# Optimization experiments

Measured on AMD Instinct MI355X. Metric: run time of the kernel, lower is better.

## Reference

```python
import jax, jax.numpy as jnp
import numpy as np

P = 64
K = 64
D = 2048
KERNEL_MUL = 2.0
KERNEL_NUM = 5


def setup_inputs() -> dict:
    key = jax.random.key(0)
    k1, k2 = jax.random.split(key)
    source = jax.random.normal(k1, (P * K, D), dtype=jnp.float32)
    target = jax.random.normal(k2, (P * K, D), dtype=jnp.float32)
    return {"source": source, "target": target}


def _mmd_terms(source, target):
    # split into P groups of K rows each, process all splits at once
    src = source.reshape(P, K, D)
    tgt = target.reshape(P, K, D)
    total = jnp.concatenate([src, tgt], axis=1)          # [P, 2K, D]
    n = 2 * K
    # pairwise squared L2 distances per split: [P, 2K, 2K]
    sq = jnp.sum(total * total, axis=-1)                  # [P, 2K]
    gram = jnp.einsum('pid,pjd->pij', total, total)       # [P, 2K, 2K]
    l2 = sq[:, :, None] + sq[:, None, :] - 2.0 * gram
    # bandwidth from detached distances (torch uses L2_distance.data)
    bw = jax.lax.stop_gradient(jnp.sum(l2, axis=(1, 2))) / (n * n - n)  # [P]
    bw = bw / (KERNEL_MUL ** (KERNEL_NUM // 2))
    mults = KERNEL_MUL ** jnp.arange(KERNEL_NUM, dtype=jnp.float32)     # [kn]
    bws = bw[:, None] * mults[None, :] + 1e-9                           # [P, kn]
    # multi-bandwidth Gaussian kernel sum: [P, 2K, 2K]
    kern = jnp.sum(jnp.exp(-l2[:, None, :, :] / bws[:, :, None, None]), axis=1)
    XX = kern[:, :K, :K]
    YY = kern[:, K:, K:]
    XY = kern[:, :K, K:]
    YX = kern[:, K:, :K]
    xx = jnp.mean(XX, axis=(1, 2))
    yy = jnp.mean(YY, axis=(1, 2))
    xy = jnp.mean(XY, axis=(1, 2))
    yx = jnp.mean(YX, axis=(1, 2))
    per_split_loss = xx + yy - xy - yx                    # [P]
    total_loss = jnp.sum(per_split_loss) / P
    return total_loss, l2, xx, yy, xy, yx


def reference(source, target):
    total_loss, l2, xx, yy, xy, yx = _mmd_terms(source, target)
    # original returns max of l2dist from the LAST split only
    max_l2_last = jnp.max(l2[-1])
    return (total_loss.reshape(1), max_l2_last,
            jnp.sum(xx) / P, jnp.sum(yy) / P, jnp.sum(xy) / P, jnp.sum(yx) / P)
```

## Files before the change

kernel.cpp:

```cpp
#include <hip/hip_runtime.h>

typedef _Float16 half8 __attribute__((ext_vector_type(8)));
typedef _Float16 half4v __attribute__((ext_vector_type(4)));
typedef float floatx4 __attribute__((ext_vector_type(4)));
typedef unsigned int uint2v __attribute__((ext_vector_type(2)));

#define NSPLIT 64
#define KS 64
#define DIM 2048
#define NROW 128
#define BK 128
#define KSPL 4
#define KCH (DIM / KSPL)
#define NKC_A (KCH / BK)
#define SST 152
#define GSZ (NROW * NROW)
#define NBLK (NSPLIT * KSPL)
#define GT2F_OFF (NBLK * GSZ / 2)
#define PART_OFF (GT2F_OFF + NBLK)
#define FLAG_OFF (PART_OFF + NBLK * 4)


__device__ __forceinline__ unsigned int pk16(float a, float b) {
  return __builtin_bit_cast(unsigned int, __builtin_amdgcn_cvt_pkrtz(a, b));
}

__global__ __launch_bounds__(1024) void gram_kernel(const float* __restrict__ src,
                                                    const float* __restrict__ tgt,
                                                    float* __restrict__ ws) {
  __shared__ __align__(16) _Float16 stage[NROW * SST];
  __shared__ float red[16];

  const int p = blockIdx.x >> 2;
  const int c = blockIdx.x & (KSPL - 1);
  const int tid = threadIdx.x;
  const int lane = tid & 63;
  const int wave = tid >> 6;

  const int srow = tid >> 3;
  const int c4 = (tid & 7) * 4;
  const float* rowp = ((srow < KS) ? (src + (size_t)(p * KS + srow) * DIM)
                                   : (tgt + (size_t)(p * KS + (srow - KS)) * DIM)) +
                      c * KCH;

  const int wr = (wave >> 2) * 32;
  const int wc = (wave & 3) * 32;
  const int fr = lane & 15;
  const int fk = (lane >> 4) * 8;

  floatx4 acc00 = {0.f, 0.f, 0.f, 0.f};
  floatx4 acc01 = {0.f, 0.f, 0.f, 0.f};
  floatx4 acc10 = {0.f, 0.f, 0.f, 0.f};
  floatx4 acc11 = {0.f, 0.f, 0.f, 0.f};

  float4 f0, f1, f2, f3;
#define LOADK(kc)                                      \
  do {                                                 \
    const float* gp_ = rowp + (kc) * BK + c4;          \
    f0 = *(const float4*)(gp_);                        \
    f1 = *(const float4*)(gp_ + 32);                   \
    f2 = *(const float4*)(gp_ + 64);                   \
    f3 = *(const float4*)(gp_ + 96);                   \
  } while (0)

  LOADK(0);
  for (int kc = 0; kc < NKC_A; ++kc) {
    __syncthreads();
    {
      _Float16* sp = &stage[srow * SST + c4];
      *(uint2v*)(sp)      = (uint2v){pk16(f0.x, f0.y), pk16(f0.z, f0.w)};
      *(uint2v*)(sp + 32) = (uint2v){pk16(f1.x, f1.y), pk16(f1.z, f1.w)};
      *(uint2v*)(sp + 64) = (uint2v){pk16(f2.x, f2.y), pk16(f2.z, f2.w)};
      *(uint2v*)(sp + 96) = (uint2v){pk16(f3.x, f3.y), pk16(f3.z, f3.w)};
    }
    __syncthreads();
    if (kc + 1 < NKC_A) LOADK(kc + 1);
#pragma unroll
    for (int ks = 0; ks < 4; ++ks) {
      const int ko = ks * 32 + fk;
      half8 a0 = *(const half8*)&stage[(wr + fr) * SST + ko];
      half8 a1 = *(const half8*)&stage[(wr + 16 + fr) * SST + ko];
      half8 b0 = *(const half8*)&stage[(wc + fr) * SST + ko];
      half8 b1 = *(const half8*)&stage[(wc + 16 + fr) * SST + ko];
      acc00 = __builtin_amdgcn_mfma_f32_16x16x32_f16(a0, b0, acc00, 0, 0, 0);
      acc01 = __builtin_amdgcn_mfma_f32_16x16x32_f16(a0, b1, acc01, 0, 0, 0);
      acc10 = __builtin_amdgcn_mfma_f32_16x16x32_f16(a1, b0, acc10, 0, 0, 0);
      acc11 = __builtin_amdgcn_mfma_f32_16x16x32_f16(a1, b1, acc11, 0, 0, 0);
    }
  }
#undef LOADK

  _Float16* hs = (_Float16*)ws + (size_t)blockIdx.x * GSZ + wave * 1024 + lane * 4;
  {
    half4v h0, h1, h2, h3;
#pragma unroll
    for (int r = 0; r < 4; ++r) {
      h0[r] = (_Float16)acc00[r];
      h1[r] = (_Float16)acc01[r];
      h2[r] = (_Float16)acc10[r];
      h3[r] = (_Float16)acc11[r];
    }
    *(half4v*)(hs)       = h0;
    *(half4v*)(hs + 256) = h1;
    *(half4v*)(hs + 512) = h2;
    *(half4v*)(hs + 768) = h3;
  }

  float gsum = 0.0f;
#pragma unroll
  for (int r = 0; r < 4; ++r) gsum += acc00[r] + acc01[r] + acc10[r] + acc11[r];
#pragma unroll
  for (int m = 1; m <= 32; m <<= 1) gsum += __shfl_xor(gsum, m, 64);
  if (lane == 0) red[wave] = gsum;
  __syncthreads();
  if (tid == 0) {
    float t = 0.0f;
    for (int w = 0; w < 16; ++w) t += red[w];
    ws[GT2F_OFF + blockIdx.x] = t;
  }
}

__global__ __launch_bounds__(1024) void reduce_kernel(float* __restrict__ ws,
                                                      float* __restrict__ out) {
  __shared__ float sqv[NROW];
  __shared__ float bcast[8];
  __shared__ float redm[16];
  __shared__ float quad2[2];
  __shared__ float fr2[4][5];
  __shared__ int sh_go;

  const int b = blockIdx.x;
  const int p = b >> 2;
  const int rb = b & 3;
  const int tid = threadIdx.x;
  const int lane = tid & 63;
  const int wave = tid >> 6;
  int* iflag = (int*)(ws + FLAG_OFF);

  const int row = rb * 32 + (tid >> 5);
  const int cg = tid & 31;

  const _Float16* sb = (const _Float16*)ws + (size_t)(p * KSPL) * GSZ;
  const int wv = ((row >> 5) << 2) + (cg >> 3);
  const int a = (((row >> 4) & 1) << 1) + ((cg >> 2) & 1);
  const int ln = (((row & 15) >> 2) << 4) + ((cg & 3) << 2);
  const int idx = wv * 1024 + a * 256 + ln * 4 + (row & 3);

  float g0 = 0.f, g1 = 0.f, g2 = 0.f, g3 = 0.f;
#pragma unroll
  for (int c8 = 0; c8 < KSPL; ++c8) {
    const _Float16* bp = sb + (size_t)c8 * GSZ + idx;
    g0 += (float)bp[0]; g1 += (float)bp[4]; g2 += (float)bp[8]; g3 += (float)bp[12];
  }

  if (tid < NROW) {
    const int i = tid;
    const int wd = (i >> 5) * 5;
    const int ad = ((i >> 4) & 1) * 3;
    const int lnd = (((i & 15) >> 2) << 4) + (i & 15);
    const int idxd = wd * 1024 + ad * 256 + lnd * 4 + (i & 3);
    float d = 0.0f;
#pragma unroll
    for (int c8 = 0; c8 < KSPL; ++c8) d += (float)sb[(size_t)c8 * GSZ + idxd];
    sqv[i] = d;
  }
  if (tid < 2) quad2[tid] = 0.0f;
  __syncthreads();

  if (tid == 0) {
    float ssq = 0.0f;
    for (int i = 0; i < NROW; ++i) ssq += sqv[i];
    float gt = ws[GT2F_OFF + p * 4 + 0] + ws[GT2F_OFF + p * 4 + 1] +
               ws[GT2F_OFF + p * 4 + 2] + ws[GT2F_OFF + p * 4 + 3];
    float suml2 = 2.0f * (float)NROW * ssq - 2.0f * gt;
    float bw = suml2 / (float)(NROW * NROW - NROW) * 0.25f;
    float mult = 1.0f;
    for (int k = 0; k < 5; ++k) {
      bcast[k] = 1.0f / (bw * mult + 1e-9f);
      mult *= 2.0f;
    }
  }
  __syncthreads();

  const float sqi = sqv[row];
  float l2r[4];
  float lmax = 0.0f;
  {
    const float gg[4] = {g0, g1, g2, g3};
#pragma unroll
    for (int k = 0; k < 4; ++k) {
      float v = sqi + sqv[cg * 4 + k] - 2.0f * gg[k];
      l2r[k] = v;
      lmax = fmaxf(lmax, v);
    }
  }
#pragma unroll
  for (int m = 1; m <= 32; m <<= 1) lmax = fmaxf(lmax, __shfl_xor(lmax, m, 64));
  if (lane == 0) redm[wave] = lmax;

  const float ib0 = bcast[0], ib1 = bcast[1], ib2 = bcast[2], ib3 = bcast[3], ib4 = bcast[4];
  float qsum = 0.0f;
#pragma unroll
  for (int k = 0; k < 4; ++k) {
    float v = l2r[k];
    qsum += __expf(-v * ib0) + __expf(-v * ib1) + __expf(-v * ib2) +
            __expf(-v * ib3) + __expf(-v * ib4);
  }
  qsum += __shfl_xor(qsum, 1, 64);
  qsum += __shfl_xor(qsum, 2, 64);
  qsum += __shfl_xor(qsum, 4, 64);
  qsum += __shfl_xor(qsum, 8, 64);
  qsum += __shfl_xor(qsum, 32, 64);
  if (lane == 0) atomicAdd(&quad2[0], qsum);
  if (lane == 16) atomicAdd(&quad2[1], qsum);
  __syncthreads();

  if (tid == 0) {
    float mx = 0.0f;
    for (int w = 0; w < 16; ++w) mx = fmaxf(mx, redm[w]);
    float4* part = (float4*)(ws + PART_OFF);
    part[b] = make_float4(quad2[0], quad2[1], mx, 0.0f);
  }

  __syncthreads();
  if (tid == 0) {
    int prev = __hip_atomic_fetch_add(&iflag[0], 1, __ATOMIC_ACQ_REL,
                                      __HIP_MEMORY_SCOPE_AGENT);
    sh_go = (prev == NBLK - 1) ? 1 : 0;
  }
  __syncthreads();
  if (!sh_go) return;

  float xx = 0.f, xy = 0.f, yx = 0.f, yy = 0.f, mx = 0.f;
  if (tid < NBLK) {
    const float4* part = (const float4*)(ws + PART_OFF);
    float4 pt = part[tid];
    int rbq = tid & 3;
    if (rbq < 2) { xx = pt.x; xy = pt.y; }
    else         { yx = pt.x; yy = pt.y; }
    if ((tid >> 2) == NSPLIT - 1) mx = pt.z;
  }
#pragma unroll
  for (int m = 1; m <= 32; m <<= 1) {
    xx += __shfl_xor(xx, m, 64);
    xy += __shfl_xor(xy, m, 64);
    yx += __shfl_xor(yx, m, 64);
    yy += __shfl_xor(yy, m, 64);
    mx = fmaxf(mx, __shfl_xor(mx, m, 64));
  }
  if (lane == 0 && wave < 4) {
    fr2[wave][0] = xx; fr2[wave][1] = xy; fr2[wave][2] = yx; fr2[wave][3] = yy; fr2[wave][4] = mx;
  }
  __syncthreads();
  if (tid == 0) {
    float sxx = 0, sxy = 0, syx = 0, syy = 0, smx = 0;
    for (int w = 0; w < 4; ++w) {
      sxx += fr2[w][0]; sxy += fr2[w][1]; syx += fr2[w][2]; syy += fr2[w][3];
      smx = fmaxf(smx, fr2[w][4]);
    }
    const float inv = 1.0f / (4096.0f * 64.0f);
    out[0] = (sxx + syy - sxy - syx) * inv;
    out[1] = smx;
    out[2] = sxx * inv;
    out[3] = syy * inv;
    out[4] = sxy * inv;
    out[5] = syx * inv;
  }
}

extern "C" void kernel_launch(void* const* d_in, const int* in_sizes, int n_in,
                              void* d_out, int out_size, void* d_ws, size_t ws_size,
                              hipStream_t stream) {
  const float* src = (const float*)d_in[0];
  const float* tgt = (const float*)d_in[1];
  float* out = (float*)d_out;
  float* ws = (float*)d_ws;
  hipMemsetAsync(ws + FLAG_OFF, 0, sizeof(int), stream);
  gram_kernel<<<NBLK, 1024, 0, stream>>>(src, tgt, ws);
  reduce_kernel<<<NBLK, 1024, 0, stream>>>(ws, out);
}
```

Before: 112.5 us.

## Double-buffer gram staging and replace last-block atomic with separate final kernel

The gram kernel now double-buffers its shared staging tile and issues the next global load before the barrier, removing one __syncthreads per k-chunk and overlapping loads with MFMA work. The reduce kernel drops the memset, atomic counter and last-block-done election, and a third single-block kernel performs the final cross-split reduction. This removes the memset launch and the atomic handshake, but adds one kernel launch and doubles the LDS used by the gram kernel. Note that reduce_kernel's ws parameter is now declared const while the kernel still writes the partials through it.

```diff
diff --git a/kernel.cpp b/kernel.cpp
--- a/kernel.cpp
+++ b/kernel.cpp
@@ -18,7 +18,6 @@
 #define NBLK (NSPLIT * KSPL)
 #define GT2F_OFF (NBLK * GSZ / 2)
 #define PART_OFF (GT2F_OFF + NBLK)
-#define FLAG_OFF (PART_OFF + NBLK * 4)
 
 
 __device__ __forceinline__ unsigned int pk16(float a, float b) {
@@ -28,7 +27,7 @@
 __global__ __launch_bounds__(1024) void gram_kernel(const float* __restrict__ src,
                                                     const float* __restrict__ tgt,
                                                     float* __restrict__ ws) {
-  __shared__ __align__(16) _Float16 stage[NROW * SST];
+  __shared__ __align__(16) _Float16 stage[2][NROW * SST];
   __shared__ float red[16];
 
   const int p = blockIdx.x >> 2;
@@ -64,24 +63,25 @@
   } while (0)
 
   LOADK(0);
+#pragma unroll
   for (int kc = 0; kc < NKC_A; ++kc) {
-    __syncthreads();
     {
-      _Float16* sp = &stage[srow * SST + c4];
+      _Float16* sp = &stage[kc & 1][srow * SST + c4];
       *(uint2v*)(sp)      = (uint2v){pk16(f0.x, f0.y), pk16(f0.z, f0.w)};
       *(uint2v*)(sp + 32) = (uint2v){pk16(f1.x, f1.y), pk16(f1.z, f1.w)};
       *(uint2v*)(sp + 64) = (uint2v){pk16(f2.x, f2.y), pk16(f2.z, f2.w)};
       *(uint2v*)(sp + 96) = (uint2v){pk16(f3.x, f3.y), pk16(f3.z, f3.w)};
     }
+    if (kc + 1 < NKC_A) LOADK(kc + 1);
     __syncthreads();
-    if (kc + 1 < NKC_A) LOADK(kc + 1);
+    const _Float16* sbuf = stage[kc & 1];
 #pragma unroll
     for (int ks = 0; ks < 4; ++ks) {
       const int ko = ks * 32 + fk;
-      half8 a0 = *(const half8*)&stage[(wr + fr) * SST + ko];
-      half8 a1 = *(const half8*)&stage[(wr + 16 + fr) * SST + ko];
-      half8 b0 = *(const half8*)&stage[(wc + fr) * SST + ko];
-      half8 b1 = *(const half8*)&stage[(wc + 16 + fr) * SST + ko];
+      half8 a0 = *(const half8*)&sbuf[(wr + fr) * SST + ko];
+      half8 a1 = *(const half8*)&sbuf[(wr + 16 + fr) * SST + ko];
+      half8 b0 = *(const half8*)&sbuf[(wc + fr) * SST + ko];
+      half8 b1 = *(const half8*)&sbuf[(wc + 16 + fr) * SST + ko];
       acc00 = __builtin_amdgcn_mfma_f32_16x16x32_f16(a0, b0, acc00, 0, 0, 0);
       acc01 = __builtin_amdgcn_mfma_f32_16x16x32_f16(a0, b1, acc01, 0, 0, 0);
       acc10 = __builtin_amdgcn_mfma_f32_16x16x32_f16(a1, b0, acc10, 0, 0, 0);
@@ -120,14 +120,12 @@
   }
 }
 
-__global__ __launch_bounds__(1024) void reduce_kernel(float* __restrict__ ws,
+__global__ __launch_bounds__(1024) void reduce_kernel(const float* __restrict__ ws,
                                                       float* __restrict__ out) {
   __shared__ float sqv[NROW];
   __shared__ float bcast[8];
   __shared__ float redm[16];
   __shared__ float quad2[2];
-  __shared__ float fr2[4][5];
-  __shared__ int sh_go;
 
   const int b = blockIdx.x;
   const int p = b >> 2;
@@ -135,7 +133,6 @@
   const int tid = threadIdx.x;
   const int lane = tid & 63;
   const int wave = tid >> 6;
-  int* iflag = (int*)(ws + FLAG_OFF);
 
   const int row = rb * 32 + (tid >> 5);
   const int cg = tid & 31;
@@ -221,25 +218,22 @@
     float4* part = (float4*)(ws + PART_OFF);
     part[b] = make_float4(quad2[0], quad2[1], mx, 0.0f);
   }
-
-  __syncthreads();
-  if (tid == 0) {
-    int prev = __hip_atomic_fetch_add(&iflag[0], 1, __ATOMIC_ACQ_REL,
-                                      __HIP_MEMORY_SCOPE_AGENT);
-    sh_go = (prev == NBLK - 1) ? 1 : 0;
-  }
-  __syncthreads();
-  if (!sh_go) return;
-
-  float xx = 0.f, xy = 0.f, yx = 0.f, yy = 0.f, mx = 0.f;
-  if (tid < NBLK) {
-    const float4* part = (const float4*)(ws + PART_OFF);
-    float4 pt = part[tid];
-    int rbq = tid & 3;
-    if (rbq < 2) { xx = pt.x; xy = pt.y; }
-    else         { yx = pt.x; yy = pt.y; }
-    if ((tid >> 2) == NSPLIT - 1) mx = pt.z;
-  }
+}
+
+__global__ __launch_bounds__(256) void final_kernel(const float* __restrict__ ws,
+                                                    float* __restrict__ out) {
+  __shared__ float fr2[4][5];
+  const int tid = threadIdx.x;
+  const int lane = tid & 63;
+  const int wave = tid >> 6;
+  const float4* part = (const float4*)(ws + PART_OFF);
+  float4 pt = part[tid];
+  const int rb = tid & 3;
+  float xx = (rb < 2) ? pt.x : 0.0f;
+  float xy = (rb < 2) ? pt.y : 0.0f;
+  float yx = (rb >= 2) ? pt.x : 0.0f;
+  float yy = (rb >= 2) ? pt.y : 0.0f;
+  float mx = ((tid >> 2) == NSPLIT - 1) ? pt.z : 0.0f;
 #pragma unroll
   for (int m = 1; m <= 32; m <<= 1) {
     xx += __shfl_xor(xx, m, 64);
@@ -248,7 +242,7 @@
     yy += __shfl_xor(yy, m, 64);
     mx = fmaxf(mx, __shfl_xor(mx, m, 64));
   }
-  if (lane == 0 && wave < 4) {
+  if (lane == 0) {
     fr2[wave][0] = xx; fr2[wave][1] = xy; fr2[wave][2] = yx; fr2[wave][3] = yy; fr2[wave][4] = mx;
   }
   __syncthreads();
@@ -275,7 +269,7 @@
   const float* tgt = (const float*)d_in[1];
   float* out = (float*)d_out;
   float* ws = (float*)d_ws;
-  hipMemsetAsync(ws + FLAG_OFF, 0, sizeof(int), stream);
   gram_kernel<<<NBLK, 1024, 0, stream>>>(src, tgt, ws);
   reduce_kernel<<<NBLK, 1024, 0, stream>>>(ws, out);
-}
+  final_kernel<<<1, 256, 0, stream>>>(ws, out);
+}
```

Measured after the change: 107.8 us. -4.2%, faster.
